# Kernel optimization log

Hardware: AMD Instinct MI355X
Metric: run time of the kernel (lower is better)

Reference implementation:

```python
import jax, jax.numpy as jnp
import numpy as np

N_NODES = 75000
N_EDGES = 1200000


def gcn_conv(x, src, dst, W, b, n):
    # linear transform first (PyG GCNConv applies lin before propagate)
    h = x @ W  # [n, out]
    # add self loops
    loop = jnp.arange(n, dtype=src.dtype)
    s = jnp.concatenate([src, loop])
    d = jnp.concatenate([dst, loop])
    # symmetric normalization: deg computed on destination after self-loops
    deg = jnp.zeros((n,), dtype=h.dtype).at[d].add(1.0)
    dinv = jnp.where(deg > 0, jax.lax.rsqrt(deg), 0.0)
    norm = dinv[s] * dinv[d]  # [E+n]
    msgs = h[s] * norm[:, None]  # gather + scale, [E+n, out]
    out = jax.ops.segment_sum(msgs, d, num_segments=n)  # scatter-add
    return out + b


def setup_inputs() -> dict:
    key = jax.random.key(0)
    ks = jax.random.split(key, 6)
    x = jax.random.normal(ks[0], (N_NODES, 64), dtype=jnp.float32)
    edge_index = jax.random.randint(ks[1], (2, N_EDGES), 0, N_NODES, dtype=jnp.int64)
    # Glorot-ish scaled weights
    W1 = jax.random.normal(ks[2], (64, 64), dtype=jnp.float32) * (1.0 / np.sqrt(64))
    b1 = jax.random.normal(ks[3], (64,), dtype=jnp.float32) * 0.01
    W2 = jax.random.normal(ks[4], (64, 16), dtype=jnp.float32) * (1.0 / np.sqrt(64))
    b2 = jax.random.normal(ks[5], (16,), dtype=jnp.float32) * 0.01
    return {"x": x, "edge_index": edge_index, "W1": W1, "b1": b1, "W2": W2, "b2": b2}


def reference(x, edge_index, W1, b1, W2, b2):
    src, dst = edge_index[0], edge_index[1]
    h = gcn_conv(x, src, dst, W1, b1, N_NODES)
    h = jax.nn.relu(h)
    # dropout is identity in eval mode
    out = gcn_conv(h, src, dst, W2, b2, N_NODES)
    return out
```

## Files before the change

### kernel.cpp

```cpp
#include <hip/hip_runtime.h>


#define NBSHIFT 9
#define BUCKET_NODES 512
#define CAP 10240
#define CHA 8192
#define TA 512
#define TB 512
#define MAXNB 160

__device__ __forceinline__ unsigned bfpack(float a, float b) {
  unsigned ua = __float_as_uint(a), ub = __float_as_uint(b);
  ua += 0x7fffu + ((ua >> 16) & 1u);
  ub += 0x7fffu + ((ub >> 16) & 1u);
  return (ua >> 16) | (ub & 0xffff0000u);
}

__global__ void kA_zero(int* __restrict__ bucketCur, int NB) {
  int i = blockIdx.x * blockDim.x + threadIdx.x;
  if (i < NB) bucketCur[i] = 0;
}

__launch_bounds__(TA)
__global__ void kA_bucket(const int* __restrict__ src, const int* __restrict__ dst,
                          int* __restrict__ bucketCur, int* __restrict__ bucketArr,
                          int NB, int E) {
  __shared__ int stage[CHA];
  __shared__ unsigned char binOf[CHA];
  __shared__ int cnt[MAXNB];
  __shared__ int off[MAXNB];
  __shared__ int gpos[MAXNB];
  __shared__ int cursor[MAXNB];
  __shared__ int scanbuf[256];
  int t = threadIdx.x;
  int e0 = blockIdx.x * CHA;

  for (int i = t; i < NB; i += TA) cnt[i] = 0;
  __syncthreads();
  for (int i = t; i < CHA; i += TA) {
    int e = e0 + i;
    if (e < E) atomicAdd(&cnt[dst[e] >> NBSHIFT], 1);
  }
  __syncthreads();
  if (t < 256) scanbuf[t] = (t < NB) ? cnt[t] : 0;
  __syncthreads();
  for (int o = 1; o < 256; o <<= 1) {
    int add = (t < 256 && t >= o) ? scanbuf[t - o] : 0;
    __syncthreads();
    if (t < 256) scanbuf[t] += add;
    __syncthreads();
  }
  if (t < NB) {
    off[t] = scanbuf[t] - cnt[t];
    cursor[t] = off[t];
    gpos[t] = (cnt[t] > 0) ? atomicAdd(&bucketCur[t], cnt[t]) : 0;
  }
  __syncthreads();
  for (int i = t; i < CHA; i += TA) {
    int e = e0 + i;
    if (e < E) {
      int d = dst[e], s = src[e];
      int b = d >> NBSHIFT;
      int p = atomicAdd(&cursor[b], 1);
      stage[p] = (s << NBSHIFT) | (d & (BUCKET_NODES - 1));
      binOf[p] = (unsigned char)b;
    }
  }
  __syncthreads();
  int total = scanbuf[255];
  for (int i = t; i < total; i += TA) {
    int b = binOf[i];
    int destIdx = gpos[b] + (i - off[b]);
    if (destIdx < CAP) bucketArr[b * CAP + destIdx] = stage[i];
  }
}

__global__ void kB_scan(const int* __restrict__ bucketCur, int* __restrict__ bucketBase,
                        int* __restrict__ rp, int NB, int N) {
  __shared__ int s[256];
  int t = threadIdx.x;
  int v = (t < NB) ? min(bucketCur[t], CAP) : 0;
  s[t] = v;
  __syncthreads();
  for (int o = 1; o < 256; o <<= 1) {
    int add = (t >= o) ? s[t - o] : 0;
    __syncthreads();
    s[t] += add;
    __syncthreads();
  }
  if (t < NB) bucketBase[t] = s[t] - v;
  if (t == NB - 1) {
    bucketBase[NB] = s[t];
    rp[N] = s[t];
  }
}

__launch_bounds__(TB)
__global__ void kB_fill(const int* __restrict__ bucketArr, const int* __restrict__ bucketCur,
                        const int* __restrict__ bucketBase,
                        int* __restrict__ rp, float* __restrict__ dinv,
                        int* __restrict__ col, int N) {
  __shared__ int hist[BUCKET_NODES];
  __shared__ int noff[BUCKET_NODES];
  __shared__ int cur[BUCKET_NODES];
  __shared__ int colStage[CAP];
  int b = blockIdx.x;
  int t = threadIdx.x;
  int nE = min(bucketCur[b], CAP);
  int base = b * CAP;

  hist[t] = 0;
  __syncthreads();
  for (int i = t; i < nE; i += TB) {
    atomicAdd(&hist[bucketArr[base + i] & (BUCKET_NODES - 1)], 1);
  }
  __syncthreads();
  int myv = hist[t];
  noff[t] = myv;
  __syncthreads();
  for (int o = 1; o < BUCKET_NODES; o <<= 1) {
    int add = (t >= o) ? noff[t - o] : 0;
    __syncthreads();
    noff[t] += add;
    __syncthreads();
  }
  int excl = noff[t] - myv;
  cur[t] = excl;
  int gnode = b * BUCKET_NODES + t;
  if (gnode < N) {
    rp[gnode] = bucketBase[b] + excl;
    dinv[gnode] = rsqrtf((float)(myv + 1));
  }
  __syncthreads();
  for (int i = t; i < nE; i += TB) {
    int v = bucketArr[base + i];
    int p = atomicAdd(&cur[v & (BUCKET_NODES - 1)], 1);
    colStage[p] = v >> NBSHIFT;
  }
  __syncthreads();
  int gb = bucketBase[b];
  for (int i = t; i < nE; i += TB) col[gb + i] = colStage[i];
}

__launch_bounds__(256)
__global__ void k_gemm64(const float4* __restrict__ X4, const float4* __restrict__ W4,
                         const float* __restrict__ dinv, uint2* __restrict__ outb,
                         int n) {
  __shared__ float4 Xs[64 * 17];
  __shared__ float4 Ws[64 * 16];
  int t = threadIdx.x;
  int base = blockIdx.x * 64;
  {
    int rr = t >> 2, q = t & 3;
    int r = base + rr;
    #pragma unroll
    for (int c = 0; c < 4; c++) {
      float4 v = make_float4(0.f, 0.f, 0.f, 0.f);
      if (r < n) v = X4[r * 16 + q * 4 + c];
      Xs[rr * 17 + q * 4 + c] = v;
      Ws[t + 256 * c] = W4[t + 256 * c];
    }
  }
  __syncthreads();

  int tx = t & 15, ty = t >> 4;
  float4 a0 = make_float4(0.f, 0.f, 0.f, 0.f), a1 = a0, a2 = a0, a3 = a0;
  #pragma unroll
  for (int kb = 0; kb < 16; kb++) {
    float4 x0 = Xs[(ty * 4 + 0) * 17 + kb];
    float4 x1 = Xs[(ty * 4 + 1) * 17 + kb];
    float4 x2 = Xs[(ty * 4 + 2) * 17 + kb];
    float4 x3 = Xs[(ty * 4 + 3) * 17 + kb];
    float4 w0 = Ws[(kb * 4 + 0) * 16 + tx];
    float4 w1 = Ws[(kb * 4 + 1) * 16 + tx];
    float4 w2 = Ws[(kb * 4 + 2) * 16 + tx];
    float4 w3 = Ws[(kb * 4 + 3) * 16 + tx];
    #define FMA4(A, XS) \
      A.x = fmaf(XS.x, w0.x, A.x); A.y = fmaf(XS.x, w0.y, A.y); \
      A.z = fmaf(XS.x, w0.z, A.z); A.w = fmaf(XS.x, w0.w, A.w); \
      A.x = fmaf(XS.y, w1.x, A.x); A.y = fmaf(XS.y, w1.y, A.y); \
      A.z = fmaf(XS.y, w1.z, A.z); A.w = fmaf(XS.y, w1.w, A.w); \
      A.x = fmaf(XS.z, w2.x, A.x); A.y = fmaf(XS.z, w2.y, A.y); \
      A.z = fmaf(XS.z, w2.z, A.z); A.w = fmaf(XS.z, w2.w, A.w); \
      A.x = fmaf(XS.w, w3.x, A.x); A.y = fmaf(XS.w, w3.y, A.y); \
      A.z = fmaf(XS.w, w3.z, A.z); A.w = fmaf(XS.w, w3.w, A.w);
    FMA4(a0, x0) FMA4(a1, x1) FMA4(a2, x2) FMA4(a3, x3)
    #undef FMA4
  }
  #pragma unroll
  for (int i = 0; i < 4; i++) {
    int r = base + ty * 4 + i;
    if (r < n) {
      float s = dinv[r];
      float4 a = (i == 0) ? a0 : (i == 1) ? a1 : (i == 2) ? a2 : a3;
      uint2 pk;
      pk.x = bfpack(a.x * s, a.y * s);
      pk.y = bfpack(a.z * s, a.w * s);
      outb[r * 16 + tx] = pk;
    }
  }
}

__launch_bounds__(256)
__global__ void k_agg64_w2(const uint2* __restrict__ hsb,
                           const int* __restrict__ rp,
                           const int* __restrict__ col,
                           const float* __restrict__ dinv,
                           const float* __restrict__ b1,
                           const float* __restrict__ W2,
                           float* __restrict__ hs2,
                           int n) {
  int lane = threadIdx.x & 63;
  int c = lane & 15;
  int sub = lane >> 4;
  int node = (blockIdx.x * blockDim.x + threadIdx.x) >> 6;
  if (node >= n) return;

  float4 b14 = ((const float4*)b1)[c];
  float w2r[16];
  #pragma unroll
  for (int i = 0; i < 16; i++) w2r[i] = W2[(sub * 16 + i) * 16 + c];

  int s0 = rp[node], s1 = rp[node + 1];
  int dt = s1 - s0 + 1;
  float ax = 0.f, ay = 0.f, az = 0.f, aw = 0.f;
  int t = sub;
  int idx0 = 0, idx1 = 0;
  if (t < dt)     idx0 = (t == 0) ? node : col[s0 + t - 1];
  if (t + 4 < dt) idx1 = col[s0 + t + 3];
  while (t < dt) {
    int cur0 = idx0, cur1 = idx1;
    bool has1 = (t + 4) < dt;
    int tn = t + 8;
    if (tn < dt)     idx0 = col[s0 + tn - 1];
    if (tn + 4 < dt) idx1 = col[s0 + tn + 3];
    uint2 u0 = hsb[cur0 * 16 + c];
    if (has1) {
      uint2 u1 = hsb[cur1 * 16 + c];
      ax += __uint_as_float(u1.x << 16);
      ay += __uint_as_float(u1.x & 0xffff0000u);
      az += __uint_as_float(u1.y << 16);
      aw += __uint_as_float(u1.y & 0xffff0000u);
    }
    ax += __uint_as_float(u0.x << 16);
    ay += __uint_as_float(u0.x & 0xffff0000u);
    az += __uint_as_float(u0.y << 16);
    aw += __uint_as_float(u0.y & 0xffff0000u);
    t = tn;
  }
  #pragma unroll
  for (int m = 16; m <= 32; m <<= 1) {
    ax += __shfl_xor(ax, m);
    ay += __shfl_xor(ay, m);
    az += __shfl_xor(az, m);
    aw += __shfl_xor(aw, m);
  }
  float dv = dinv[node];
  float hx = fmaxf(ax * dv + b14.x, 0.f);
  float hy = fmaxf(ay * dv + b14.y, 0.f);
  float hz = fmaxf(az * dv + b14.z, 0.f);
  float hw = fmaxf(aw * dv + b14.w, 0.f);

  float part = 0.f;
  #pragma unroll
  for (int i = 0; i < 16; i++) {
    int srcLane = 4 * sub + (i >> 2);
    float h;
    if ((i & 3) == 0)      h = __shfl(hx, srcLane);
    else if ((i & 3) == 1) h = __shfl(hy, srcLane);
    else if ((i & 3) == 2) h = __shfl(hz, srcLane);
    else                   h = __shfl(hw, srcLane);
    part = fmaf(h, w2r[i], part);
  }
  #pragma unroll
  for (int m = 16; m <= 32; m <<= 1) part += __shfl_xor(part, m);
  if (sub == 0) hs2[node * 16 + c] = part * dv;
}

__launch_bounds__(256)
__global__ void k_agg16(const float4* __restrict__ hs2_4,
                        const int* __restrict__ rp,
                        const int* __restrict__ col,
                        const float* __restrict__ dinv,
                        const float* __restrict__ b2,
                        float4* __restrict__ out4,
                        int n) {
  int lane = threadIdx.x & 63;
  int c = lane & 3;
  int sub = lane >> 2;
  int node = (blockIdx.x * blockDim.x + threadIdx.x) >> 6;
  if (node >= n) return;

  int s0 = rp[node], s1 = rp[node + 1];
  int dt = s1 - s0 + 1;
  float ax = 0.f, ay = 0.f, az = 0.f, aw = 0.f;
  int t = sub;
  int idx = 0;
  if (t < dt) idx = (t == 0) ? node : col[s0 + t - 1];
  while (t < dt) {
    int curi = idx;
    int tn = t + 16;
    if (tn < dt) idx = col[s0 + tn - 1];
    float4 row = hs2_4[curi * 4 + c];
    ax += row.x; ay += row.y; az += row.z; aw += row.w;
    t = tn;
  }
  #pragma unroll
  for (int m = 4; m <= 32; m <<= 1) {
    ax += __shfl_xor(ax, m);
    ay += __shfl_xor(ay, m);
    az += __shfl_xor(az, m);
    aw += __shfl_xor(aw, m);
  }
  if (sub == 0) {
    float dv = dinv[node];
    float4 b24 = ((const float4*)b2)[c];
    float4 o;
    o.x = ax * dv + b24.x;
    o.y = ay * dv + b24.y;
    o.z = az * dv + b24.z;
    o.w = aw * dv + b24.w;
    out4[node * 4 + c] = o;
  }
}

extern "C" void kernel_launch(void* const* d_in, const int* in_sizes, int n_in,
                              void* d_out, int out_size, void* d_ws, size_t ws_size,
                              hipStream_t stream) {
  const float* x  = (const float*)d_in[0];
  const int* edges = (const int*)d_in[1];
  const float* W1 = (const float*)d_in[2];
  const float* b1 = (const float*)d_in[3];
  const float* W2 = (const float*)d_in[4];
  const float* b2 = (const float*)d_in[5];
  float* out = (float*)d_out;

  const int N = in_sizes[0] / 64;
  const int E = in_sizes[1] / 2;
  const int* src = edges;
  const int* dst = edges + E;
  const int NB = (N + BUCKET_NODES - 1) >> NBSHIFT;

  auto align = [](size_t v) { return (v + 255) & ~(size_t)255; };
  char* p = (char*)d_ws;
  float* dinv       = (float*)p; p += align((size_t)N * 4);
  int*   rp         = (int*)p;   p += align((size_t)(N + 1) * 4);
  int*   bucketCur  = (int*)p;   p += align((size_t)MAXNB * 4);
  int*   bucketBase = (int*)p;   p += align((size_t)(MAXNB + 1) * 4);
  int*   col        = (int*)p;   p += align((size_t)E * 4);
  float* hs1        = (float*)p; p += align((size_t)N * 64 * 4);
  float* hs2        = (float*)p; p += align((size_t)N * 16 * 4);
  int* bucketArr = (int*)hs1;

  const int nbA = (E + CHA - 1) / CHA;
  const int nbWave = ((size_t)N * 64 + 255) / 256;

  kA_zero  <<<(NB + 255) / 256, 256, 0, stream>>>(bucketCur, NB);
  kA_bucket<<<nbA, TA, 0, stream>>>(src, dst, bucketCur, bucketArr, NB, E);
  kB_scan  <<<1, 256, 0, stream>>>(bucketCur, bucketBase, rp, NB, N);
  kB_fill  <<<NB, TB, 0, stream>>>(bucketArr, bucketCur, bucketBase, rp, dinv, col, N);

  k_gemm64  <<<(N + 63) / 64, 256, 0, stream>>>((const float4*)x, (const float4*)W1,
                                                dinv, (uint2*)hs1, N);
  k_agg64_w2<<<nbWave, 256, 0, stream>>>((const uint2*)hs1, rp, col, dinv,
                                         b1, W2, hs2, N);
  k_agg16   <<<nbWave, 256, 0, stream>>>((const float4*)hs2, rp, col, dinv,
                                         b2, (float4*)out, N);
}
```

Before: 133.4 us.

## Store layer-2 features as bf16 and deepen gather unrolling in aggregations

The layer-1 aggregation now packs the 16-wide layer-2 features into bf16 pairs, which halves both the hs2 write and the second aggregation's gathers. Both aggregation loops now keep more independent index loads and row gathers in flight per iteration: four per lane in the 64-wide kernel and two in the 16-wide kernel. The zeroing kernel is replaced by hipMemsetAsync. bf16 storage of hs2 adds rounding error to the final output, and the deeper unrolling raises register pressure.

```diff
diff --git a/kernel.cpp b/kernel.cpp
--- a/kernel.cpp
+++ b/kernel.cpp
@@ -14,11 +14,6 @@
   ua += 0x7fffu + ((ua >> 16) & 1u);
   ub += 0x7fffu + ((ub >> 16) & 1u);
   return (ua >> 16) | (ub & 0xffff0000u);
-}
-
-__global__ void kA_zero(int* __restrict__ bucketCur, int NB) {
-  int i = blockIdx.x * blockDim.x + threadIdx.x;
-  if (i < NB) bucketCur[i] = 0;
 }
 
 __launch_bounds__(TA)
@@ -208,7 +203,7 @@
                            const float* __restrict__ dinv,
                            const float* __restrict__ b1,
                            const float* __restrict__ W2,
-                           float* __restrict__ hs2,
+                           unsigned* __restrict__ hs2b,
                            int n) {
   int lane = threadIdx.x & 63;
   int c = lane & 15;
@@ -225,27 +220,31 @@
   int dt = s1 - s0 + 1;
   float ax = 0.f, ay = 0.f, az = 0.f, aw = 0.f;
   int t = sub;
-  int idx0 = 0, idx1 = 0;
-  if (t < dt)     idx0 = (t == 0) ? node : col[s0 + t - 1];
-  if (t + 4 < dt) idx1 = col[s0 + t + 3];
+  int i0 = 0, i1 = 0, i2 = 0, i3 = 0;
+  if (t < dt)      i0 = (t == 0) ? node : col[s0 + t - 1];
+  if (t + 4 < dt)  i1 = col[s0 + t + 3];
+  if (t + 8 < dt)  i2 = col[s0 + t + 7];
+  if (t + 12 < dt) i3 = col[s0 + t + 11];
   while (t < dt) {
-    int cur0 = idx0, cur1 = idx1;
-    bool has1 = (t + 4) < dt;
-    int tn = t + 8;
-    if (tn < dt)     idx0 = col[s0 + tn - 1];
-    if (tn + 4 < dt) idx1 = col[s0 + tn + 3];
-    uint2 u0 = hsb[cur0 * 16 + c];
-    if (has1) {
-      uint2 u1 = hsb[cur1 * 16 + c];
-      ax += __uint_as_float(u1.x << 16);
-      ay += __uint_as_float(u1.x & 0xffff0000u);
-      az += __uint_as_float(u1.y << 16);
-      aw += __uint_as_float(u1.y & 0xffff0000u);
-    }
-    ax += __uint_as_float(u0.x << 16);
-    ay += __uint_as_float(u0.x & 0xffff0000u);
-    az += __uint_as_float(u0.y << 16);
-    aw += __uint_as_float(u0.y & 0xffff0000u);
+    int c0 = i0, c1 = i1, c2 = i2, c3 = i3;
+    bool h1 = (t + 4) < dt, h2 = (t + 8) < dt, h3 = (t + 12) < dt;
+    int tn = t + 16;
+    if (tn < dt)      i0 = col[s0 + tn - 1];
+    if (tn + 4 < dt)  i1 = col[s0 + tn + 3];
+    if (tn + 8 < dt)  i2 = col[s0 + tn + 7];
+    if (tn + 12 < dt) i3 = col[s0 + tn + 11];
+    uint2 u0 = hsb[c0 * 16 + c];
+    uint2 u1 = h1 ? hsb[c1 * 16 + c] : make_uint2(0u, 0u);
+    uint2 u2 = h2 ? hsb[c2 * 16 + c] : make_uint2(0u, 0u);
+    uint2 u3 = h3 ? hsb[c3 * 16 + c] : make_uint2(0u, 0u);
+    ax += __uint_as_float(u0.x << 16) + __uint_as_float(u1.x << 16)
+        + __uint_as_float(u2.x << 16) + __uint_as_float(u3.x << 16);
+    ay += __uint_as_float(u0.x & 0xffff0000u) + __uint_as_float(u1.x & 0xffff0000u)
+        + __uint_as_float(u2.x & 0xffff0000u) + __uint_as_float(u3.x & 0xffff0000u);
+    az += __uint_as_float(u0.y << 16) + __uint_as_float(u1.y << 16)
+        + __uint_as_float(u2.y << 16) + __uint_as_float(u3.y << 16);
+    aw += __uint_as_float(u0.y & 0xffff0000u) + __uint_as_float(u1.y & 0xffff0000u)
+        + __uint_as_float(u2.y & 0xffff0000u) + __uint_as_float(u3.y & 0xffff0000u);
     t = tn;
   }
   #pragma unroll
@@ -274,11 +273,15 @@
   }
   #pragma unroll
   for (int m = 16; m <= 32; m <<= 1) part += __shfl_xor(part, m);
-  if (sub == 0) hs2[node * 16 + c] = part * dv;
+  part *= dv;
+  float pnext = __shfl_down(part, 1);
+  if (sub == 0 && (c & 1) == 0) {
+    hs2b[node * 8 + (c >> 1)] = bfpack(part, pnext);
+  }
 }
 
 __launch_bounds__(256)
-__global__ void k_agg16(const float4* __restrict__ hs2_4,
+__global__ void k_agg16(const uint2* __restrict__ hs2b,
                         const int* __restrict__ rp,
                         const int* __restrict__ col,
                         const float* __restrict__ dinv,
@@ -295,14 +298,21 @@
   int dt = s1 - s0 + 1;
   float ax = 0.f, ay = 0.f, az = 0.f, aw = 0.f;
   int t = sub;
-  int idx = 0;
-  if (t < dt) idx = (t == 0) ? node : col[s0 + t - 1];
+  int i0 = 0, i1 = 0;
+  if (t < dt)      i0 = (t == 0) ? node : col[s0 + t - 1];
+  if (t + 16 < dt) i1 = col[s0 + t + 15];
   while (t < dt) {
-    int curi = idx;
-    int tn = t + 16;
-    if (tn < dt) idx = col[s0 + tn - 1];
-    float4 row = hs2_4[curi * 4 + c];
-    ax += row.x; ay += row.y; az += row.z; aw += row.w;
+    int c0 = i0, c1 = i1;
+    bool h1 = (t + 16) < dt;
+    int tn = t + 32;
+    if (tn < dt)      i0 = col[s0 + tn - 1];
+    if (tn + 16 < dt) i1 = col[s0 + tn + 15];
+    uint2 u0 = hs2b[c0 * 4 + c];
+    uint2 u1 = h1 ? hs2b[c1 * 4 + c] : make_uint2(0u, 0u);
+    ax += __uint_as_float(u0.x << 16) + __uint_as_float(u1.x << 16);
+    ay += __uint_as_float(u0.x & 0xffff0000u) + __uint_as_float(u1.x & 0xffff0000u);
+    az += __uint_as_float(u0.y << 16) + __uint_as_float(u1.y << 16);
+    aw += __uint_as_float(u0.y & 0xffff0000u) + __uint_as_float(u1.y & 0xffff0000u);
     t = tn;
   }
   #pragma unroll
@@ -355,7 +365,7 @@
   const int nbA = (E + CHA - 1) / CHA;
   const int nbWave = ((size_t)N * 64 + 255) / 256;
 
-  kA_zero  <<<(NB + 255) / 256, 256, 0, stream>>>(bucketCur, NB);
+  hipMemsetAsync(bucketCur, 0, (size_t)MAXNB * 4, stream);
   kA_bucket<<<nbA, TA, 0, stream>>>(src, dst, bucketCur, bucketArr, NB, E);
   kB_scan  <<<1, 256, 0, stream>>>(bucketCur, bucketBase, rp, NB, N);
   kB_fill  <<<NB, TB, 0, stream>>>(bucketArr, bucketCur, bucketBase, rp, dinv, col, N);
@@ -363,7 +373,7 @@
   k_gemm64  <<<(N + 63) / 64, 256, 0, stream>>>((const float4*)x, (const float4*)W1,
                                                 dinv, (uint2*)hs1, N);
   k_agg64_w2<<<nbWave, 256, 0, stream>>>((const uint2*)hs1, rp, col, dinv,
-                                         b1, W2, hs2, N);
-  k_agg16   <<<nbWave, 256, 0, stream>>>((const float4*)hs2, rp, col, dinv,
+                                         b1, W2, (unsigned*)hs2, N);
+  k_agg16   <<<nbWave, 256, 0, stream>>>((const uint2*)hs2, rp, col, dinv,
                                          b2, (float4*)out, N);
 }
```

Result: faster. 129.8 us (-2.8%).
